# Kernel tuning notes

Measured on AMD Instinct MI355X. Metric: run time of the kernel, lower is better.

## Reference

```python
import jax, jax.numpy as jnp
import numpy as np

VOCAB, N_CLASS, H, E = 50000, 6, 512, 300
B, S = 256, 512


def setup_inputs() -> dict:
    key = jax.random.key(0)
    ks = jax.random.split(key, 10)
    return {
        "seq": jax.random.randint(ks[0], (B, S), 0, VOCAB),
        "classes": jnp.arange(N_CLASS),
        "embed_W": jax.random.normal(ks[1], (VOCAB, E), jnp.float32) * 0.1,
        "embed_class_W": jax.random.normal(ks[2], (N_CLASS, H), jnp.float32) * 0.1,
        "W_ih": jax.random.normal(ks[3], (3 * H, E), jnp.float32) * 0.05,
        "W_hh": jax.random.normal(ks[4], (3 * H, H), jnp.float32) * 0.05,
        "b_ih": jax.random.normal(ks[5], (3 * H,), jnp.float32) * 0.05,
        "b_hh": jax.random.normal(ks[6], (3 * H,), jnp.float32) * 0.05,
        "attend": jax.random.normal(ks[7], (H, H), jnp.float32) * 0.1,
        "W_cls": jax.random.normal(ks[8], (2, H), jnp.float32) * 0.05,
        "b_cls": jax.random.normal(ks[9], (2,), jnp.float32) * 0.05,
    }


def _gru_scan(xs, W_ih, W_hh, b_ih, b_hh):
    # xs: [S, B, E]; torch GRUCell semantics
    h0 = jnp.zeros((xs.shape[1], W_hh.shape[1]), xs.dtype)

    def step(h, x):
        gi = x @ W_ih.T + b_ih            # [B, 3H]
        gh = h @ W_hh.T + b_hh            # [B, 3H]
        i_r, i_z, i_n = jnp.split(gi, 3, axis=-1)
        h_r, h_z, h_n = jnp.split(gh, 3, axis=-1)
        r = jax.nn.sigmoid(i_r + h_r)
        z = jax.nn.sigmoid(i_z + h_z)
        n = jnp.tanh(i_n + r * h_n)
        h_new = (1.0 - z) * n + z * h
        return h_new, h_new

    _, hs = jax.lax.scan(step, h0, xs)
    return hs  # [S, B, H]


def reference(seq, classes, embed_W, embed_class_W, W_ih, W_hh, b_ih, b_hh,
              attend, W_cls, b_cls):
    pad_mask = (seq > 0).astype(embed_W.dtype)          # [B, S]
    seq_emb = jnp.tanh(embed_W[seq])                    # [B, S, E]
    hs = _gru_scan(seq_emb.transpose(1, 0, 2), W_ih, W_hh, b_ih, b_hh)
    seq_repr = hs.transpose(1, 0, 2)                    # [B, S, H]

    class_emb = embed_class_W[classes]                  # [C, H]
    attn = jnp.tanh(class_emb) @ attend                 # [C, H]
    # scores[c,b,s] = tanh(attn)[c] . seq_repr[b,s], masked
    scores = jnp.einsum('ch,bsh->cbs', jnp.tanh(attn), seq_repr)
    scores = scores * pad_mask[None, :, :]
    ctx = jnp.einsum('cbs,bsh->cbh', jnp.tanh(scores), seq_repr)  # [C, B, H]
    logits = jnp.tanh(ctx) @ W_cls.T + b_cls            # [C, B, 2]
    return jax.nn.log_softmax(logits, axis=-1)
```

## Files before the change

kernel.cpp:

```cpp
#include <hip/hip_runtime.h>
#include <cstdint>
#include <cstddef>

#define NB 256
#define NS 512
#define NE 300
#define NH 512

using f32x4 = __attribute__((ext_vector_type(4))) float;
using s16x8 = __attribute__((ext_vector_type(8))) short;

static __device__ __forceinline__ unsigned short f2bf(float f) {
  unsigned u = __float_as_uint(f);
  u += 0x7FFFu + ((u >> 16) & 1u);
  return (unsigned short)(u >> 16);
}
static __device__ __forceinline__ float bf2f(unsigned short h) {
  return __uint_as_float(((unsigned)h) << 16);
}
static __device__ __forceinline__ float fast_tanh(float x) {
  float xc = fminf(fmaxf(x, -9.f), 9.f);
  float e = __expf(2.f * xc);
  return (e - 1.f) / (e + 1.f);
}
static __device__ __forceinline__ float sigm(float x) {
  return 1.f / (1.f + __expf(-x));
}

__global__ void k_zero(unsigned short* __restrict__ h_ex, unsigned* __restrict__ flags) {
  int i = blockIdx.x * 256 + threadIdx.x;
  unsigned long long* p = (unsigned long long*)(h_ex + (size_t)i * 16);
  #pragma unroll
  for (int j = 0; j < 4; ++j)
    __hip_atomic_store(p + j, 0ull, __ATOMIC_RELAXED, __HIP_MEMORY_SCOPE_AGENT);
  if (i < 4096)
    __hip_atomic_store(flags + i, 0u, __ATOMIC_RELAXED, __HIP_MEMORY_SCOPE_AGENT);
}

__global__ __launch_bounds__(256) void k_xemb(const int* __restrict__ seq,
                                              const float* __restrict__ embed_W,
                                              unsigned short* __restrict__ x_pre) {
  const long long total = (long long)NB * NS * 40;
  for (long long t = (long long)blockIdx.x * 256 + threadIdx.x; t < total;
       t += (long long)gridDim.x * 256) {
    int c = (int)(t % 40);
    long long p = t / 40;
    int s = (int)(p % NS);
    int b = (int)(p / NS);
    int g_b = b >> 4, r = b & 15;
    float vals[8];
    if (c < 38) {
      int id = seq[(size_t)b * NS + s];
      const float* ep = embed_W + (size_t)id * NE;
      if (c < 37) {
        f32x4 u0 = *(const f32x4*)(ep + c * 8);
        f32x4 u1 = *(const f32x4*)(ep + c * 8 + 4);
        vals[0]=u0[0];vals[1]=u0[1];vals[2]=u0[2];vals[3]=u0[3];
        vals[4]=u1[0];vals[5]=u1[1];vals[6]=u1[2];vals[7]=u1[3];
      } else {
        #pragma unroll
        for (int jj = 0; jj < 8; ++jj) { int cc = 296 + jj; vals[jj] = (cc < NE) ? ep[cc] : 0.f; }
      }
    } else {
      #pragma unroll
      for (int jj = 0; jj < 8; ++jj) vals[jj] = 0.f;
    }
    s16x8 pv;
    #pragma unroll
    for (int jj = 0; jj < 8; ++jj) pv[jj] = (short)f2bf(fast_tanh(vals[jj]));
    *(s16x8*)(x_pre + (((size_t)g_b * NS + s) * 16 + r) * 320 + c * 8) = pv;
  }
}

__global__ __launch_bounds__(256) void k_amat(const int* __restrict__ classes,
                                              const float* __restrict__ ecw,
                                              const float* __restrict__ attend,
                                              unsigned short* __restrict__ a_bf) {
  __shared__ float tc[6][512];
  const int tid = threadIdx.x, j = blockIdx.x;
  for (int i = tid; i < 6 * 512; i += 256) {
    int c = i >> 9, hp = i & 511;
    tc[c][hp] = fast_tanh(ecw[(size_t)classes[c] * 512 + hp]);
  }
  __syncthreads();
  #pragma unroll
  for (int i = 0; i < 4; ++i) {
    int task = tid + 256 * i;
    int c = task >> 6, hl = task & 63;
    int h = j * 64 + hl;
    float v = 0.f;
    if (c < 6) {
      float acc = 0.f;
      for (int hp = 0; hp < 512; ++hp) acc += tc[c][hp] * attend[(size_t)hp * 512 + h];
      v = fast_tanh(acc);
    }
    a_bf[c * 512 + h] = f2bf(v);
  }
}

__global__ __launch_bounds__(448) void k_gru(
    const int* __restrict__ seq, const float* __restrict__ embed_W,
    const float* __restrict__ W_ih, const float* __restrict__ W_hh,
    const float* __restrict__ b_ih, const float* __restrict__ b_hh,
    unsigned short* __restrict__ h_ex, unsigned* __restrict__ flags,
    unsigned short* __restrict__ seq_repr,
    const unsigned short* __restrict__ x_pre, int xpre)
{
  __shared__ unsigned short x_lds[2][16][328];
  __shared__ unsigned short h_lds[16][520];
  __shared__ float rz_lds[2][16][32];

  const int tid = threadIdx.x;
  const int w = tid >> 6, l = tid & 63, lo = l & 15, hi = l >> 4;
  const bool cw = (w < 6);
  const int bid = blockIdx.x;
  const int g_b = (bid & 7) * 2 + (bid >> 7);
  const int g_c = (bid >> 3) & 15;

  const int gg = (w < 6) ? (w >> 1) : 0;
  const int cb = (w & 1) * 16;
  const int jrow = cw ? (gg * 512 + g_c * 32 + cb + lo) : 0;

  s16x8 whh[16];
  s16x8 wih[10];
  float bsum = 0.f, bni = 0.f, bnh = 0.f;
  if (cw) {
    #pragma unroll
    for (int kt = 0; kt < 16; ++kt) {
      const float* p = W_hh + (size_t)jrow * 512 + kt * 32 + hi * 8;
      f32x4 a0 = *(const f32x4*)p;
      f32x4 a1 = *(const f32x4*)(p + 4);
      s16x8 v;
      v[0]=(short)f2bf(a0[0]); v[1]=(short)f2bf(a0[1]); v[2]=(short)f2bf(a0[2]); v[3]=(short)f2bf(a0[3]);
      v[4]=(short)f2bf(a1[0]); v[5]=(short)f2bf(a1[1]); v[6]=(short)f2bf(a1[2]); v[7]=(short)f2bf(a1[3]);
      whh[kt] = v;
    }
    #pragma unroll
    for (int kt = 0; kt < 10; ++kt) {
      s16x8 v;
      #pragma unroll
      for (int jj = 0; jj < 8; ++jj) {
        int k = kt * 32 + hi * 8 + jj;
        float f = (k < NE) ? W_ih[(size_t)jrow * NE + k] : 0.f;
        v[jj] = (short)f2bf(f);
      }
      wih[kt] = v;
    }
    bsum = b_ih[jrow] + b_hh[jrow];
    bni = b_ih[jrow]; bnh = b_hh[jrow];
  }

  float hcar[4] = {0.f, 0.f, 0.f, 0.f};
  const unsigned* flg = flags + g_b * 32;

  const int xt = tid - 64;
  const bool xw = (w >= 1 && w < 6);
  const int xr0 = xw ? (xt / 40) : 0,          xc0 = xw ? (xt % 40) : 0;
  const int xr1 = xw ? ((xt + 320) / 40) : 0,  xc1 = xw ? ((xt + 320) % 40) : 0;

  auto do_gather = [&](int ss) {
    const int buf = ss & 1;
    #pragma unroll
    for (int i = 0; i < 2; ++i) {
      int task = tid + 448 * i;
      if (task < 640) {
        int r = task & 15, grp = task >> 4;
        float vals[8];
        if (grp < 38) {
          int id = seq[(size_t)(g_b * 16 + r) * NS + ss];
          const float* ep = embed_W + (size_t)id * NE;
          if (grp < 37) {
            f32x4 u0 = *(const f32x4*)(ep + grp * 8);
            f32x4 u1 = *(const f32x4*)(ep + grp * 8 + 4);
            vals[0]=u0[0];vals[1]=u0[1];vals[2]=u0[2];vals[3]=u0[3];
            vals[4]=u1[0];vals[5]=u1[1];vals[6]=u1[2];vals[7]=u1[3];
          } else {
            #pragma unroll
            for (int jj = 0; jj < 8; ++jj) { int cc = 296 + jj; vals[jj] = (cc < NE) ? ep[cc] : 0.f; }
          }
        } else {
          #pragma unroll
          for (int jj = 0; jj < 8; ++jj) vals[jj] = 0.f;
        }
        s16x8 pv;
        #pragma unroll
        for (int jj = 0; jj < 8; ++jj) pv[jj] = (short)f2bf(fast_tanh(vals[jj]));
        *(s16x8*)&x_lds[buf][r][grp * 8] = pv;
      }
    }
  };

  if (xpre) {
    if (xw) {
      const unsigned short* src = x_pre + ((size_t)g_b * NS + 0) * (16 * 320);
      s16x8 v0 = *(const s16x8*)(src + xr0 * 320 + xc0 * 8);
      s16x8 v1 = *(const s16x8*)(src + xr1 * 320 + xc1 * 8);
      *(s16x8*)&x_lds[0][xr0][xc0 * 8] = v0;
      *(s16x8*)&x_lds[0][xr1][xc1 * 8] = v1;
    }
  } else {
    do_gather(0);
  }
  __syncthreads();

  #pragma unroll 1
  for (int s = 0; s < NS; ++s) {
    if (!cw) {
      if (s > 0) {
        const unsigned* fp = flg + (l & 31);
        int guard = 0;
        for (;;) {
          unsigned f = __hip_atomic_load(fp, __ATOMIC_RELAXED, __HIP_MEMORY_SCOPE_AGENT);
          if (__all(f >= (unsigned)s)) break;
          if (++guard > (1 << 22)) break;
        }
      }
    } else {
      const bool xpf = xpre && (s + 1 < NS) && xw;
      s16x8 xv0, xv1;
      if (xpf) {
        const unsigned short* src = x_pre + ((size_t)g_b * NS + (s + 1)) * (16 * 320);
        xv0 = *(const s16x8*)(src + xr0 * 320 + xc0 * 8);
        xv1 = *(const s16x8*)(src + xr1 * 320 + xc1 * 8);
      } else if (!xpre && s + 1 < NS) {
        do_gather(s + 1);
      }
      f32x4 ax_ = {0.f,0.f,0.f,0.f};
      #pragma unroll
      for (int kt = 0; kt < 10; ++kt) {
        s16x8 af = *(const s16x8*)&x_lds[s & 1][lo][kt * 32 + hi * 8];
        ax_ = __builtin_amdgcn_mfma_f32_16x16x32_bf16(af, wih[kt], ax_, 0, 0, 0);
      }
      __syncthreads();

      const unsigned short* hsrc = h_ex + ((size_t)(s & 1) * 16 + g_b) * (16 * 512);
      #pragma unroll
      for (int i = 0; i < 5; ++i) {
        int task = tid + 448 * i;
        if (task < 2048) {
          int r = task >> 7, c4 = task & 127;
          unsigned long long v = __hip_atomic_load(
              (const unsigned long long*)(hsrc + r * 512 + c4 * 4),
              __ATOMIC_RELAXED, __HIP_MEMORY_SCOPE_AGENT);
          *(unsigned long long*)&h_lds[r][c4 * 4] = v;
        }
      }
      __syncthreads();

      if (xpf) {
        *(s16x8*)&x_lds[(s + 1) & 1][xr0][xc0 * 8] = xv0;
        *(s16x8*)&x_lds[(s + 1) & 1][xr1][xc1 * 8] = xv1;
      }

      f32x4 ah0 = {0.f,0.f,0.f,0.f}, ah1 = {0.f,0.f,0.f,0.f};
      #pragma unroll
      for (int kt = 0; kt < 16; kt += 2) {
        s16x8 af0 = *(const s16x8*)&h_lds[lo][kt * 32 + hi * 8];
        s16x8 af1 = *(const s16x8*)&h_lds[lo][(kt + 1) * 32 + hi * 8];
        ah0 = __builtin_amdgcn_mfma_f32_16x16x32_bf16(af0, whh[kt], ah0, 0, 0, 0);
        ah1 = __builtin_amdgcn_mfma_f32_16x16x32_bf16(af1, whh[kt + 1], ah1, 0, 0, 0);
      }
      f32x4 ah = ah0 + ah1;

      if (w < 4) {
        #pragma unroll
        for (int j = 0; j < 4; ++j) {
          int row = hi * 4 + j;
          rz_lds[gg][row][cb + lo] = ax_[j] + ah[j] + bsum;
        }
      }
      __syncthreads();

      if (w >= 4) {
        unsigned short* hdst = h_ex + ((size_t)((s + 1) & 1) * 16 + g_b) * (16 * 512);
        const int cpr = cb + lo;
        const int col = g_c * 32 + cpr;
        unsigned words[4];
        #pragma unroll
        for (int j = 0; j < 4; ++j) {
          int row = hi * 4 + j;
          float rr = sigm(rz_lds[0][row][cpr]);
          float zz = sigm(rz_lds[1][row][cpr]);
          float nn = fast_tanh(ax_[j] + bni + rr * (ah[j] + bnh));
          float hn = (1.f - zz) * nn + zz * hcar[j];
          hcar[j] = hn;
          unsigned myb = (unsigned)f2bf(hn);
          unsigned other = __shfl_xor(myb, 1);
          words[j] = myb | (other << 16);
        }
        if ((lo & 1) == 0) {
          #pragma unroll
          for (int j = 0; j < 4; ++j)
            __hip_atomic_store((unsigned*)(hdst + (hi * 4 + j) * 512 + col), words[j],
                               __ATOMIC_RELAXED, __HIP_MEMORY_SCOPE_AGENT);
        }
        asm volatile("s_waitcnt vmcnt(0)" ::: "memory");
        if (l == 0)
          __hip_atomic_store((unsigned*)(flags + g_b * 32 + g_c * 2 + (w & 1)),
                             (unsigned)(s + 1),
                             __ATOMIC_RELAXED, __HIP_MEMORY_SCOPE_AGENT);
        if ((lo & 1) == 0) {
          #pragma unroll
          for (int j = 0; j < 4; ++j)
            *(unsigned*)(seq_repr + ((size_t)(g_b * 16 + hi * 4 + j) * NS + s) * NH + col) = words[j];
        }
      }
      continue;
    }

    __syncthreads();
    {
      const unsigned short* hsrc = h_ex + ((size_t)(s & 1) * 16 + g_b) * (16 * 512);
      #pragma unroll
      for (int i = 0; i < 5; ++i) {
        int task = tid + 448 * i;
        if (task < 2048) {
          int r = task >> 7, c4 = task & 127;
          unsigned long long v = __hip_atomic_load(
              (const unsigned long long*)(hsrc + r * 512 + c4 * 4),
              __ATOMIC_RELAXED, __HIP_MEMORY_SCOPE_AGENT);
          *(unsigned long long*)&h_lds[r][c4 * 4] = v;
        }
      }
    }
    __syncthreads();
    __syncthreads();
  }

}

__global__ __launch_bounds__(256) void k_attn(const int* __restrict__ seq,
                                              const unsigned short* __restrict__ seq_repr,
                                              const unsigned short* __restrict__ a_bf,
                                              const float* __restrict__ W_cls,
                                              const float* __restrict__ b_cls,
                                              float* __restrict__ out)
{
  __shared__ unsigned short V[32][520];
  __shared__ float P[32][8];
  __shared__ float red[4][12];
  const int tid = threadIdx.x, b = blockIdx.x;
  const int w = tid >> 6, l = tid & 63, lo = l & 15, hi = l >> 4;

  s16x8 afr[16];
  #pragma unroll
  for (int kt = 0; kt < 16; ++kt)
    afr[kt] = *(const s16x8*)(a_bf + (size_t)lo * 512 + kt * 32 + hi * 8);

  float ctx0[6] = {0,0,0,0,0,0}, ctx1[6] = {0,0,0,0,0,0};
  const unsigned short* vbase = seq_repr + (size_t)b * NS * NH;

  for (int sc = 0; sc < 16; ++sc) {
    #pragma unroll 4
    for (int i = 0; i < 8; ++i) {
      int task = tid + 256 * i;
      int sl = task >> 6, grp = task & 63;
      s16x8 v = *(const s16x8*)(vbase + (size_t)(sc * 32 + sl) * NH + grp * 8);
      *(s16x8*)&V[sl][grp * 8] = v;
    }
    __syncthreads();
    if (w < 2) {
      f32x4 acc = {0.f,0.f,0.f,0.f};
      int sl0 = w * 16;
      #pragma unroll
      for (int kt = 0; kt < 16; ++kt) {
        s16x8 af = *(const s16x8*)&V[sl0 + lo][kt * 32 + hi * 8];
        acc = __builtin_amdgcn_mfma_f32_16x16x32_bf16(af, afr[kt], acc, 0, 0, 0);
      }
      if (lo < 8) {
        #pragma unroll
        for (int j = 0; j < 4; ++j) {
          int sl = sl0 + hi * 4 + j;
          float p = 0.f;
          if (lo < 6) {
            int s = sc * 32 + sl;
            p = (seq[(size_t)b * NS + s] > 0) ? fast_tanh(acc[j]) : 0.f;
          }
          P[sl][lo] = p;
        }
      }
    }
    __syncthreads();
    #pragma unroll 2
    for (int sl = 0; sl < 32; ++sl) {
      unsigned v2 = *(const unsigned*)&V[sl][tid * 2];
      float v0 = bf2f((unsigned short)(v2 & 0xFFFFu));
      float v1 = bf2f((unsigned short)(v2 >> 16));
      #pragma unroll
      for (int c = 0; c < 6; ++c) {
        float p = P[sl][c];
        ctx0[c] += p * v0; ctx1[c] += p * v1;
      }
    }
    __syncthreads();
  }

  float pl[12];
  #pragma unroll
  for (int c = 0; c < 6; ++c) {
    float t0 = fast_tanh(ctx0[c]), t1 = fast_tanh(ctx1[c]);
    pl[c * 2 + 0] = t0 * W_cls[tid * 2] + t1 * W_cls[tid * 2 + 1];
    pl[c * 2 + 1] = t0 * W_cls[512 + tid * 2] + t1 * W_cls[512 + tid * 2 + 1];
  }
  #pragma unroll
  for (int i = 0; i < 12; ++i) {
    float v = pl[i];
    for (int off = 32; off > 0; off >>= 1) v += __shfl_down(v, off);
    if (l == 0) red[w][i] = v;
  }
  __syncthreads();
  if (tid < 6) {
    int c = tid;
    float l0 = red[0][c*2] + red[1][c*2] + red[2][c*2] + red[3][c*2] + b_cls[0];
    float l1 = red[0][c*2+1] + red[1][c*2+1] + red[2][c*2+1] + red[3][c*2+1] + b_cls[1];
    float m = fmaxf(l0, l1);
    float lse = m + logf(__expf(l0 - m) + __expf(l1 - m));
    out[c * 512 + b * 2 + 0] = l0 - lse;
    out[c * 512 + b * 2 + 1] = l1 - lse;
  }
}

extern "C" void kernel_launch(void* const* d_in, const int* in_sizes, int n_in,
                              void* d_out, int out_size, void* d_ws, size_t ws_size,
                              hipStream_t stream) {
  const int*   seq      = (const int*)d_in[0];
  const int*   classes  = (const int*)d_in[1];
  const float* embed_W  = (const float*)d_in[2];
  const float* ecw      = (const float*)d_in[3];
  const float* W_ih     = (const float*)d_in[4];
  const float* W_hh     = (const float*)d_in[5];
  const float* b_ih     = (const float*)d_in[6];
  const float* b_hh     = (const float*)d_in[7];
  const float* attend   = (const float*)d_in[8];
  const float* W_cls    = (const float*)d_in[9];
  const float* b_cls    = (const float*)d_in[10];
  float* out = (float*)d_out;

  char* ws = (char*)d_ws;
  const size_t OFF_HEX  = 134217728;
  const size_t OFF_FLG  = OFF_HEX + 524288;
  const size_t OFF_ABF  = OFF_FLG + 16384;
  const size_t OFF_XPRE = OFF_ABF + 16384;
  const size_t XPRE_BYTES = (size_t)16 * NS * 16 * 320 * 2;
  unsigned short* seq_repr = (unsigned short*)ws;
  unsigned short* h_ex     = (unsigned short*)(ws + OFF_HEX);
  unsigned*       flags    = (unsigned*)(ws + OFF_FLG);
  unsigned short* a_bf     = (unsigned short*)(ws + OFF_ABF);
  unsigned short* x_pre    = (unsigned short*)(ws + OFF_XPRE);
  const int xpre = (ws_size >= OFF_XPRE + XPRE_BYTES) ? 1 : 0;

  hipLaunchKernelGGL(k_zero, dim3(64), dim3(256), 0, stream, h_ex, flags);
  hipLaunchKernelGGL(k_amat, dim3(8), dim3(256), 0, stream, classes, ecw, attend, a_bf);
  if (xpre)
    hipLaunchKernelGGL(k_xemb, dim3(2048), dim3(256), 0, stream, seq, embed_W, x_pre);
  hipLaunchKernelGGL(k_gru, dim3(256), dim3(448), 0, stream,
                     seq, embed_W, W_ih, W_hh, b_ih, b_hh, h_ex, flags, seq_repr,
                     x_pre, xpre);
  hipLaunchKernelGGL(k_attn, dim3(256), dim3(256), 0, stream,
                     seq, seq_repr, a_bf, W_cls, b_cls, out);
}
```

Before: 2.152 ms.

## Stream per-slice GRU hidden-state loads using LDS readiness mask from poller waves

The poller wave now publishes a ballot bitmask of which producer slices have written their new hidden-state chunk into a shared LDS word. Compute waves spin on that word and load each 32-column slice of h as soon as its two producers are ready, instead of waiting for a full-block barrier after all flags arrive. The h-fetch work moves to the six compute waves using a slice-aligned task mapping, and the extra barriers in the poller path are removed. This adds LDS spin loops with iteration guards, and it depends on the mask reset and double buffering being correctly ordered against the barrier.

```diff
diff --git a/kernel.cpp b/kernel.cpp
--- a/kernel.cpp
+++ b/kernel.cpp
@@ -109,6 +109,7 @@
   __shared__ unsigned short x_lds[2][16][328];
   __shared__ unsigned short h_lds[16][520];
   __shared__ float rz_lds[2][16][32];
+  __shared__ unsigned rdy[2];
 
   const int tid = threadIdx.x;
   const int w = tid >> 6, l = tid & 63, lo = l & 15, hi = l >> 4;
@@ -158,11 +159,14 @@
   const int xr0 = xw ? (xt / 40) : 0,          xc0 = xw ? (xt % 40) : 0;
   const int xr1 = xw ? ((xt + 320) / 40) : 0,  xc1 = xw ? ((xt + 320) % 40) : 0;
 
+  const int sp = tid & 15;
+  const int t24 = tid >> 4;
+
   auto do_gather = [&](int ss) {
     const int buf = ss & 1;
     #pragma unroll
     for (int i = 0; i < 2; ++i) {
-      int task = tid + 448 * i;
+      int task = tid + 384 * i;
       if (task < 640) {
         int r = task & 15, grp = task >> 4;
         float vals[8];
@@ -198,26 +202,18 @@
       *(s16x8*)&x_lds[0][xr0][xc0 * 8] = v0;
       *(s16x8*)&x_lds[0][xr1][xc1 * 8] = v1;
     }
-  } else {
+  } else if (cw) {
     do_gather(0);
   }
   __syncthreads();
 
   #pragma unroll 1
   for (int s = 0; s < NS; ++s) {
-    if (!cw) {
-      if (s > 0) {
-        const unsigned* fp = flg + (l & 31);
-        int guard = 0;
-        for (;;) {
-          unsigned f = __hip_atomic_load(fp, __ATOMIC_RELAXED, __HIP_MEMORY_SCOPE_AGENT);
-          if (__all(f >= (unsigned)s)) break;
-          if (++guard > (1 << 22)) break;
-        }
-      }
-    } else {
-      const bool xpf = xpre && (s + 1 < NS) && xw;
-      s16x8 xv0, xv1;
+    const bool xpf = xpre && (s + 1 < NS) && xw;
+    s16x8 xv0, xv1;
+    f32x4 ax_ = {0.f,0.f,0.f,0.f};
+
+    if (cw) {
       if (xpf) {
         const unsigned short* src = x_pre + ((size_t)g_b * NS + (s + 1)) * (16 * 320);
         xv0 = *(const s16x8*)(src + xr0 * 320 + xc0 * 8);
@@ -225,33 +221,73 @@
       } else if (!xpre && s + 1 < NS) {
         do_gather(s + 1);
       }
-      f32x4 ax_ = {0.f,0.f,0.f,0.f};
       #pragma unroll
       for (int kt = 0; kt < 10; ++kt) {
         s16x8 af = *(const s16x8*)&x_lds[s & 1][lo][kt * 32 + hi * 8];
         ax_ = __builtin_amdgcn_mfma_f32_16x16x32_bf16(af, wih[kt], ax_, 0, 0, 0);
       }
-      __syncthreads();
-
+    } else {
+      if (s > 0) {
+        const unsigned* fp = flg + (l & 31);
+        int guard = 0; unsigned last = 0;
+        for (;;) {
+          unsigned f = __hip_atomic_load(fp, __ATOMIC_RELAXED, __HIP_MEMORY_SCOPE_AGENT);
+          unsigned m32 = (unsigned)__ballot(f >= (unsigned)s);
+          if (l == 0 && m32 != last) {
+            __hip_atomic_store(&rdy[s & 1], m32, __ATOMIC_RELEASE, __HIP_MEMORY_SCOPE_WORKGROUP);
+            last = m32;
+          }
+          if (m32 == 0xFFFFFFFFu) break;
+          if (++guard > (1 << 12)) {
+            if (l == 0)
+              __hip_atomic_store(&rdy[s & 1], 0xFFFFFFFFu, __ATOMIC_RELEASE, __HIP_MEMORY_SCOPE_WORKGROUP);
+            break;
+          }
+        }
+      }
+    }
+
+    if (cw) {
       const unsigned short* hsrc = h_ex + ((size_t)(s & 1) * 16 + g_b) * (16 * 512);
-      #pragma unroll
-      for (int i = 0; i < 5; ++i) {
-        int task = tid + 448 * i;
-        if (task < 2048) {
-          int r = task >> 7, c4 = task & 127;
-          unsigned long long v = __hip_atomic_load(
+      if (s > 0) {
+        const int p2 = sp * 2;
+        int g2 = 0;
+        for (;;) {
+          unsigned m = __hip_atomic_load(&rdy[s & 1], __ATOMIC_ACQUIRE, __HIP_MEMORY_SCOPE_WORKGROUP);
+          if (((m >> p2) & 3u) == 3u) break;
+          if (++g2 > (1 << 14)) break;
+        }
+      }
+      unsigned long long hv[6];
+      #pragma unroll
+      for (int k = 0; k < 6; ++k) {
+        int j = t24 + 24 * k;
+        if (j < 128) {
+          int r = j >> 3, c4 = sp * 8 + (j & 7);
+          hv[k] = __hip_atomic_load(
               (const unsigned long long*)(hsrc + r * 512 + c4 * 4),
               __ATOMIC_RELAXED, __HIP_MEMORY_SCOPE_AGENT);
-          *(unsigned long long*)&h_lds[r][c4 * 4] = v;
-        }
-      }
-      __syncthreads();
-
+        }
+      }
+      #pragma unroll
+      for (int k = 0; k < 6; ++k) {
+        int j = t24 + 24 * k;
+        if (j < 128) {
+          int r = j >> 3, c4 = sp * 8 + (j & 7);
+          *(unsigned long long*)&h_lds[r][c4 * 4] = hv[k];
+        }
+      }
+    }
+    __syncthreads();
+
+    if (!cw) {
+      if (l == 0)
+        __hip_atomic_store(&rdy[(s + 1) & 1], 0u, __ATOMIC_RELAXED, __HIP_MEMORY_SCOPE_WORKGROUP);
+    } else {
       if (xpf) {
         *(s16x8*)&x_lds[(s + 1) & 1][xr0][xc0 * 8] = xv0;
         *(s16x8*)&x_lds[(s + 1) & 1][xr1][xc1 * 8] = xv1;
       }
-
       f32x4 ah0 = {0.f,0.f,0.f,0.f}, ah1 = {0.f,0.f,0.f,0.f};
       #pragma unroll
       for (int kt = 0; kt < 16; kt += 2) {
@@ -287,11 +323,8 @@
           unsigned myb = (unsigned)f2bf(hn);
           unsigned other = __shfl_xor(myb, 1);
           words[j] = myb | (other << 16);
-        }
-        if ((lo & 1) == 0) {
-          #pragma unroll
-          for (int j = 0; j < 4; ++j)
-            __hip_atomic_store((unsigned*)(hdst + (hi * 4 + j) * 512 + col), words[j],
+          if ((lo & 1) == 0)
+            __hip_atomic_store((unsigned*)(hdst + row * 512 + col), words[j],
                                __ATOMIC_RELAXED, __HIP_MEMORY_SCOPE_AGENT);
         }
         asm volatile("s_waitcnt vmcnt(0)" ::: "memory");
@@ -307,26 +340,8 @@
       }
       continue;
     }
-
     __syncthreads();
-    {
-      const unsigned short* hsrc = h_ex + ((size_t)(s & 1) * 16 + g_b) * (16 * 512);
-      #pragma unroll
-      for (int i = 0; i < 5; ++i) {
-        int task = tid + 448 * i;
-        if (task < 2048) {
-          int r = task >> 7, c4 = task & 127;
-          unsigned long long v = __hip_atomic_load(
-              (const unsigned long long*)(hsrc + r * 512 + c4 * 4),
-              __ATOMIC_RELAXED, __HIP_MEMORY_SCOPE_AGENT);
-          *(unsigned long long*)&h_lds[r][c4 * 4] = v;
-        }
-      }
-    }
-    __syncthreads();
-    __syncthreads();
-  }
-
+  }
 }
 
 __global__ __launch_bounds__(256) void k_attn(const int* __restrict__ seq,
```

Measured after the change: 2.053 ms, median of 2. 4.6% less time.
